# Kernel optimization log

Hardware: AMD Instinct MI355X
Metric: run time of the kernel (lower is better)

## Reference

```python
import jax, jax.numpy as jnp
import numpy as np

DIM = 768
N_HEADS = 12
HEAD_DIM = DIM // N_HEADS
HIDDEN = int(DIM * 4.0)
EPS = 1e-6


def setup_inputs() -> dict:
    key = jax.random.key(0)
    ks = jax.random.split(key, 12)
    s = 0.02
    return {
        "x": jax.random.normal(ks[0], (4, 2048, DIM), dtype=jnp.float32),
        "ln1_g": jnp.ones((DIM,), jnp.float32),
        "ln1_b": jnp.zeros((DIM,), jnp.float32),
        "qkv_w": jax.random.normal(ks[1], (3 * DIM, DIM), jnp.float32) * s,
        "qkv_b": jnp.zeros((3 * DIM,), jnp.float32),
        "proj_w": jax.random.normal(ks[2], (DIM, DIM), jnp.float32) * s,
        "proj_b": jnp.zeros((DIM,), jnp.float32),
        "ln2_g": jnp.ones((DIM,), jnp.float32),
        "ln2_b": jnp.zeros((DIM,), jnp.float32),
        "fc1_w": jax.random.normal(ks[3], (HIDDEN, DIM), jnp.float32) * s,
        "fc1_b": jnp.zeros((HIDDEN,), jnp.float32),
        "fc2_w": jax.random.normal(ks[4], (DIM, HIDDEN), jnp.float32) * s,
        "fc2_b": jnp.zeros((DIM,), jnp.float32),
    }


def layer_norm(x, g, b):
    mu = jnp.mean(x, axis=-1, keepdims=True)
    var = jnp.mean(jnp.square(x - mu), axis=-1, keepdims=True)
    return (x - mu) * jax.lax.rsqrt(var + EPS) * g + b


def reference(x, ln1_g, ln1_b, qkv_w, qkv_b, proj_w, proj_b,
              ln2_g, ln2_b, fc1_w, fc1_b, fc2_w, fc2_b):
    B, N, D = x.shape
    # --- attention branch ---
    h = layer_norm(x, ln1_g, ln1_b)
    qkv = h @ qkv_w.T + qkv_b                      # [B, N, 3D]
    qkv = qkv.reshape(B, N, 3, N_HEADS, HEAD_DIM).transpose(2, 0, 3, 1, 4)
    q, k, v = qkv[0], qkv[1], qkv[2]               # each [B, H, N, d]
    scale = HEAD_DIM ** -0.5
    scores = jnp.einsum("bhqd,bhkd->bhqk", q, k) * scale
    attn = jax.nn.softmax(scores, axis=-1)
    out = jnp.einsum("bhqk,bhkd->bhqd", attn, v)   # [B, H, N, d]
    out = out.transpose(0, 2, 1, 3).reshape(B, N, D)
    x = x + (out @ proj_w.T + proj_b)
    # --- MLP branch ---
    h = layer_norm(x, ln2_g, ln2_b)
    h = jax.nn.gelu(h @ fc1_w.T + fc1_b, approximate=False)
    x = x + (h @ fc2_w.T + fc2_b)
    return x
```

## Files before the change

kernel.cpp:

```cpp
#include <hip/hip_runtime.h>


#define DIM    768
#define NHEAD  12
#define HDIM   64
#define HID    3072
#define BATCH  4
#define SEQ    2048
#define MTOT   (BATCH * SEQ)
#define D3     (3 * DIM)

#define QSCALE 0.18033688011112042f
#define GELU_K 2.30220816f

typedef short bf16x8 __attribute__((ext_vector_type(8)));
typedef float f32x4  __attribute__((ext_vector_type(4)));

__device__ __forceinline__ float exp2fast(float x) {
    return __builtin_amdgcn_exp2f(x);
}

__device__ __forceinline__ float gelu_f(float v) {
    float y = v * (1.f + 0.044715f * v * v) * GELU_K;
    float t = exp2fast(fminf(y, 30.f));
#if __has_builtin(__builtin_amdgcn_rcpf)
    return v * t * __builtin_amdgcn_rcpf(t + 1.f);
#else
    return v * t / (t + 1.f);
#endif
}

__device__ __forceinline__ short f2bf(float f) {
    union { float f; unsigned u; } c; c.f = f;
    unsigned r = c.u + 0x7FFFu + ((c.u >> 16) & 1u);
    return (short)(r >> 16);
}

__device__ __forceinline__ short4 pk4bf(float a, float b, float c, float d) {
#if __has_builtin(__builtin_amdgcn_cvt_pk_bf16_f32)
    auto lo = __builtin_amdgcn_cvt_pk_bf16_f32(a, b);
    auto hi = __builtin_amdgcn_cvt_pk_bf16_f32(c, d);
    union { decltype(lo) v; int i; } ul, uh;
    ul.v = lo; uh.v = hi;
    short4 r;
    *(int*)&r.x = ul.i; *(int*)&r.z = uh.i;
    return r;
#else
    return make_short4(f2bf(a), f2bf(b), f2bf(c), f2bf(d));
#endif
}

__device__ __forceinline__ void gld_lds16(const short* g, short* l) {
    __builtin_amdgcn_global_load_lds(
        (const __attribute__((address_space(1))) unsigned int*)g,
        (__attribute__((address_space(3))) unsigned int*)l, 16, 0, 0);
}

__global__ __launch_bounds__(256) void tobf4_k(
    const float* __restrict__ s0, short* __restrict__ d0, int n0,
    const float* __restrict__ s1, short* __restrict__ d1, int n1,
    const float* __restrict__ s2, short* __restrict__ d2, int n2,
    const float* __restrict__ s3, short* __restrict__ d3, int n3)
{
    int i = blockIdx.x * 256 + threadIdx.x;
    const float* s; short* d;
    if (i < n0)                { s = s0; d = d0; }
    else if ((i -= n0) < n1)   { s = s1; d = d1; }
    else if ((i -= n1) < n2)   { s = s2; d = d2; }
    else if ((i -= n2) < n3)   { s = s3; d = d3; }
    else return;
    float4 v = ((const float4*)s)[i];
    ((short4*)d)[i] = pk4bf(v.x, v.y, v.z, v.w);
}

__global__ __launch_bounds__(256) void ln_k(
    const float* __restrict__ x, const float* __restrict__ g,
    const float* __restrict__ bta, short* __restrict__ y)
{
    __shared__ float sb[2][4];
    const int row = blockIdx.x, tid = threadIdx.x;
    const float* xr = x + (size_t)row * DIM;
    float v0 = xr[tid], v1 = xr[tid + 256], v2 = xr[tid + 512];
    float s = v0 + v1 + v2;
    #pragma unroll
    for (int o = 32; o; o >>= 1) s += __shfl_down(s, o);
    if ((tid & 63) == 0) sb[0][tid >> 6] = s;
    __syncthreads();
    float mu = (sb[0][0] + sb[0][1] + sb[0][2] + sb[0][3]) * (1.f / DIM);
    float d0 = v0 - mu, d1 = v1 - mu, d2 = v2 - mu;
    float q = d0 * d0 + d1 * d1 + d2 * d2;
    #pragma unroll
    for (int o = 32; o; o >>= 1) q += __shfl_down(q, o);
    if ((tid & 63) == 0) sb[1][tid >> 6] = q;
    __syncthreads();
    float var = (sb[1][0] + sb[1][1] + sb[1][2] + sb[1][3]) * (1.f / DIM);
    float inv = rsqrtf(var + 1e-6f);
    short* yr = y + (size_t)row * DIM;
    yr[tid]       = f2bf(d0 * inv * g[tid]       + bta[tid]);
    yr[tid + 256] = f2bf(d1 * inv * g[tid + 256] + bta[tid + 256]);
    yr[tid + 512] = f2bf(d2 * inv * g[tid + 512] + bta[tid + 512]);
}

template<int BN, int WM, int WN, int TM, int TN, int MODE>
__global__ __launch_bounds__(256) void gemm_bt(
    const short* __restrict__ A, const short* __restrict__ W,
    const float* __restrict__ bias, const float* __restrict__ resid,
    void* __restrict__ Cout, short* __restrict__ vt,
    int M, int N, int K)
{
    __shared__ __align__(16) short smem[2 * 128 * 32 + 2 * BN * 32];
    short (*A0)[32] = (short(*)[32])smem;
    short (*A1)[32] = (short(*)[32])(smem + 128 * 32);
    short (*B0)[32] = (short(*)[32])(smem + 2 * 128 * 32);
    short (*B1)[32] = (short(*)[32])(smem + 2 * 128 * 32 + BN * 32);

    const int tid = threadIdx.x, lane = tid & 63, wv = tid >> 6;
    const int bm = blockIdx.y << 7;
    const int bn = blockIdx.x * BN;
    const int wmo = (wv / WN) * (TM * 16);
    const int wno = (wv % WN) * (TN * 16);
    const int l15 = lane & 15, quad = lane >> 4;

    const int srow = lane >> 2;
    const int scol = (lane & 3) << 3;

    f32x4 acc[TM][TN] = {};

    for (int k0 = 0; k0 < K; k0 += 64) {
        __syncthreads();
        #pragma unroll
        for (int p = 0; p < 2; ++p) {
            const int rs = wv * 16 + p * 64;
            const short* ga = A + (size_t)(bm + rs + srow) * K + k0 + scol;
            gld_lds16(ga,      &A0[rs][0]);
            gld_lds16(ga + 32, &A1[rs][0]);
        }
        #pragma unroll
        for (int p = 0; p < BN / 64; ++p) {
            const int rs = wv * 16 + p * 64;
            const short* gw = W + (size_t)(bn + rs + srow) * K + k0 + scol;
            gld_lds16(gw,      &B0[rs][0]);
            gld_lds16(gw + 32, &B1[rs][0]);
        }
        __syncthreads();

        #pragma unroll
        for (int ks = 0; ks < 2; ++ks) {
            short (*As)[32] = ks ? A1 : A0;
            short (*Bs)[32] = ks ? B1 : B0;
            bf16x8 af[TM], bfr[TN];
            #pragma unroll
            for (int t = 0; t < TM; ++t)
                af[t] = *(const bf16x8*)&As[wmo + t * 16 + l15][quad << 3];
            #pragma unroll
            for (int u = 0; u < TN; ++u)
                bfr[u] = *(const bf16x8*)&Bs[wno + u * 16 + l15][quad << 3];
            #pragma unroll
            for (int t = 0; t < TM; ++t)
                #pragma unroll
                for (int u = 0; u < TN; ++u)
                    acc[t][u] = __builtin_amdgcn_mfma_f32_16x16x32_bf16(
                        af[t], bfr[u], acc[t][u], 0, 0, 0);
        }
    }

    if (MODE == 3 && bn >= 1536) {
        short (*Tr)[136] = (short(*)[136])smem;
        #pragma unroll 1
        for (int half = 0; half < 2; ++half) {
            __syncthreads();
            if ((wno >> 6) == half) {
                #pragma unroll
                for (int u = 0; u < TN; ++u) {
                    const float bv = bias[bn + half * 64 + u * 16 + l15];
                    #pragma unroll
                    for (int t = 0; t < TM; ++t)
                        *(short4*)&Tr[u * 16 + l15][wmo + t * 16 + (quad << 2)] =
                            pk4bf(acc[t][u][0] + bv, acc[t][u][1] + bv,
                                  acc[t][u][2] + bv, acc[t][u][3] + bv);
                }
            }
            __syncthreads();
            const int dd = tid >> 2, seg = (tid & 3) << 5;
            const int col = bn + half * 64 + dd;
            const int hh = (col - 1536) >> 6, d = (col - 1536) & 63;
            const int b = bm >> 11, n0 = (bm & 2047) + seg;
            short* dst = &vt[((((size_t)b * NHEAD + hh) << 6) + d) * SEQ + n0];
            #pragma unroll
            for (int c = 0; c < 4; ++c)
                ((int4*)dst)[c] = *(const int4*)&Tr[dd][seg + (c << 3)];
        }
        return;
    }

    #pragma unroll
    for (int u = 0; u < TN; ++u) {
        const int col = bn + wno + u * 16 + l15;
        const float bv = bias[col];
        #pragma unroll
        for (int t = 0; t < TM; ++t) {
            const int row0 = bm + wmo + t * 16 + (quad << 2);
            #pragma unroll
            for (int r = 0; r < 4; ++r) {
                float v = acc[t][u][r] + bv;
                const size_t idx = (size_t)(row0 + r) * N + col;
                if (MODE == 0) {
                    ((float*)Cout)[idx] = v + resid[idx];
                } else if (MODE == 2) {
                    ((short*)Cout)[idx] = f2bf(gelu_f(v));
                } else {
                    if (col < DIM) v *= QSCALE;
                    ((short*)Cout)[idx] = f2bf(v);
                }
            }
        }
    }
}

__global__ __launch_bounds__(256) void attn_k(
    const short* __restrict__ qkv, const short* __restrict__ vt,
    short* __restrict__ out)
{
    __shared__ __align__(16) short Ks[64][72];
    __shared__ __align__(16) short Vs[64][72];
    __shared__ __align__(16) short Ps[4][32][72];

    const int bh = blockIdx.x, b = bh / NHEAD, h = bh % NHEAD;
    const int qb = blockIdx.y;
    const int tid = threadIdx.x, lane = tid & 63, wv = tid >> 6;
    const int l15 = lane & 15, quad = lane >> 4;

    const size_t qbase = (size_t)b * SEQ * D3;
    const size_t vbase = (((size_t)bh) << 6) * SEQ;

    bf16x8 qf[2][2];
    #pragma unroll
    for (int tm = 0; tm < 2; ++tm) {
        const int m = (qb << 7) + wv * 32 + tm * 16 + l15;
        #pragma unroll
        for (int ks = 0; ks < 2; ++ks)
            qf[tm][ks] = *(const bf16x8*)&qkv[qbase + (size_t)m * D3 + h * HDIM
                                             + ks * 32 + (quad << 3)];
    }

    float psum[2] = {0.f, 0.f};
    f32x4 acc[2][4] = {};

    const int srow = tid >> 3;
    const int scol = (tid & 7) << 3;

    for (int kb = 0; kb < SEQ / 64; ++kb) {
        __syncthreads();
        #pragma unroll
        for (int p = 0; p < 2; ++p) {
            const int r = srow + p * 32;
            *(int4*)&Ks[r][scol] = *(const int4*)&qkv[qbase
                + (size_t)((kb << 6) + r) * D3 + DIM + h * HDIM + scol];
            *(int4*)&Vs[r][scol] = *(const int4*)&vt[vbase
                + (size_t)r * SEQ + (kb << 6) + scol];
        }
        __syncthreads();

        f32x4 st[2][4] = {};
        #pragma unroll
        for (int kt = 0; kt < 4; ++kt)
            #pragma unroll
            for (int ks = 0; ks < 2; ++ks) {
                bf16x8 kf = *(const bf16x8*)&Ks[kt * 16 + l15][ks * 32 + (quad << 3)];
                #pragma unroll
                for (int tm = 0; tm < 2; ++tm)
                    st[tm][kt] = __builtin_amdgcn_mfma_f32_16x16x32_bf16(
                        kf, qf[tm][ks], st[tm][kt], 0, 0, 0);
            }

        #pragma unroll
        for (int tm = 0; tm < 2; ++tm) {
            #pragma unroll
            for (int kt = 0; kt < 4; ++kt) {
                const float p0 = exp2fast(st[tm][kt][0]);
                const float p1 = exp2fast(st[tm][kt][1]);
                const float p2 = exp2fast(st[tm][kt][2]);
                const float p3 = exp2fast(st[tm][kt][3]);
                psum[tm] += (p0 + p1) + (p2 + p3);
                *(short4*)&Ps[wv][tm * 16 + l15][kt * 16 + (quad << 2)] =
                    pk4bf(p0, p1, p2, p3);
            }
        }

        #pragma unroll
        for (int ks = 0; ks < 2; ++ks) {
            bf16x8 pf[2];
            #pragma unroll
            for (int tm = 0; tm < 2; ++tm)
                pf[tm] = *(const bf16x8*)&Ps[wv][tm * 16 + l15][ks * 32 + (quad << 3)];
            #pragma unroll
            for (int u = 0; u < 4; ++u) {
                bf16x8 vf = *(const bf16x8*)&Vs[u * 16 + l15][ks * 32 + (quad << 3)];
                #pragma unroll
                for (int tm = 0; tm < 2; ++tm)
                    acc[tm][u] = __builtin_amdgcn_mfma_f32_16x16x32_bf16(
                        vf, pf[tm], acc[tm][u], 0, 0, 0);
            }
        }
    }

    #pragma unroll
    for (int tm = 0; tm < 2; ++tm) {
        psum[tm] += __shfl_xor(psum[tm], 16);
        psum[tm] += __shfl_xor(psum[tm], 32);
    }

    #pragma unroll
    for (int tm = 0; tm < 2; ++tm) {
        const float inv = 1.f / psum[tm];
        const int q = (qb << 7) + wv * 32 + tm * 16 + l15;
        #pragma unroll
        for (int u = 0; u < 4; ++u) {
            const int d0 = u * 16 + (quad << 2);
            *(short4*)&out[((size_t)b * SEQ + q) * DIM + h * HDIM + d0] =
                pk4bf(acc[tm][u][0] * inv, acc[tm][u][1] * inv,
                      acc[tm][u][2] * inv, acc[tm][u][3] * inv);
        }
    }
}

extern "C" void kernel_launch(void* const* d_in, const int* in_sizes, int n_in,
                              void* d_out, int out_size, void* d_ws, size_t ws_size,
                              hipStream_t stream) {
    const float* x      = (const float*)d_in[0];
    const float* ln1_g  = (const float*)d_in[1];
    const float* ln1_b  = (const float*)d_in[2];
    const float* qkv_w  = (const float*)d_in[3];
    const float* qkv_b  = (const float*)d_in[4];
    const float* proj_w = (const float*)d_in[5];
    const float* proj_b = (const float*)d_in[6];
    const float* ln2_g  = (const float*)d_in[7];
    const float* ln2_b  = (const float*)d_in[8];
    const float* fc1_w  = (const float*)d_in[9];
    const float* fc1_b  = (const float*)d_in[10];
    const float* fc2_w  = (const float*)d_in[11];
    const float* fc2_b  = (const float*)d_in[12];
    float* out = (float*)d_out;

    short* ws16 = (short*)d_ws;
    short* wqkv = ws16;
    short* wprj = wqkv + (size_t)D3 * DIM;
    short* wf1  = wprj + (size_t)DIM * DIM;
    short* wf2  = wf1  + (size_t)HID * DIM;
    short* h    = wf2  + (size_t)DIM * HID;
    short* big  = h    + (size_t)MTOT * DIM;
    short* vtb  = big  + (size_t)MTOT * HID;
    float* x2   = (float*)(vtb + (size_t)MTOT * DIM);

    dim3 blk(256);

    const int n0 = (D3 * DIM) / 4, n1 = (DIM * DIM) / 4,
              n2 = (HID * DIM) / 4, n3 = (DIM * HID) / 4;
    tobf4_k<<<(n0 + n1 + n2 + n3 + 255) / 256, blk, 0, stream>>>(
        qkv_w, wqkv, n0, proj_w, wprj, n1, fc1_w, wf1, n2, fc2_w, wf2, n3);

    ln_k<<<MTOT, blk, 0, stream>>>(x, ln1_g, ln1_b, h);
    gemm_bt<128, 2, 2, 4, 4, 3><<<dim3(D3 / 128, MTOT / 128), blk, 0, stream>>>(
        h, wqkv, qkv_b, nullptr, big, vtb, MTOT, D3, DIM);
    attn_k<<<dim3(BATCH * NHEAD, SEQ / 128), blk, 0, stream>>>(big, vtb, h);
    gemm_bt<64, 4, 1, 2, 4, 0><<<dim3(DIM / 64, MTOT / 128), blk, 0, stream>>>(
        h, wprj, proj_b, x, x2, nullptr, MTOT, DIM, DIM);
    ln_k<<<MTOT, blk, 0, stream>>>(x2, ln2_g, ln2_b, vtb);
    gemm_bt<128, 2, 2, 4, 4, 2><<<dim3(HID / 128, MTOT / 128), blk, 0, stream>>>(
        vtb, wf1, fc1_b, nullptr, big, nullptr, MTOT, HID, DIM);
    gemm_bt<64, 4, 1, 2, 4, 0><<<dim3(DIM / 64, MTOT / 128), blk, 0, stream>>>(
        big, wf2, fc2_b, x2, out, nullptr, MTOT, DIM, HID);
}
```

Measured before the change: 431.1 us.

## Replace GEMM with 256x128-tile, 8-wave, double-buffered swizzled-LDS kernel

Replaces the templated 128xBN GEMM with a single 512-thread kernel that computes 256x128 output tiles. It double-buffers LDS so the next K-slice loads while MFMAs run, and XOR-swizzles the LDS layout to avoid bank conflicts. It also raises wave priority around MFMA issue. The V-transpose epilogue now writes short4 directly from registers instead of staging through LDS. The risks are lower occupancy from 96KB of LDS per block, and fewer blocks for the 768-wide projection GEMMs (only 6x32 tiles), which could hurt load balance.

```diff
diff --git a/kernel.cpp b/kernel.cpp
--- a/kernel.cpp
+++ b/kernel.cpp
@@ -37,17 +37,12 @@
 }
 
 __device__ __forceinline__ short4 pk4bf(float a, float b, float c, float d) {
-#if __has_builtin(__builtin_amdgcn_cvt_pk_bf16_f32)
-    auto lo = __builtin_amdgcn_cvt_pk_bf16_f32(a, b);
-    auto hi = __builtin_amdgcn_cvt_pk_bf16_f32(c, d);
-    union { decltype(lo) v; int i; } ul, uh;
-    ul.v = lo; uh.v = hi;
+    int lo, hi;
+    asm("v_cvt_pk_bf16_f32 %0, %1, %2" : "=v"(lo) : "v"(a), "v"(b));
+    asm("v_cvt_pk_bf16_f32 %0, %1, %2" : "=v"(hi) : "v"(c), "v"(d));
     short4 r;
-    *(int*)&r.x = ul.i; *(int*)&r.z = uh.i;
+    *(int*)&r.x = lo; *(int*)&r.z = hi;
     return r;
-#else
-    return make_short4(f2bf(a), f2bf(b), f2bf(c), f2bf(d));
-#endif
 }
 
 __device__ __forceinline__ void gld_lds16(const short* g, short* l) {
@@ -101,108 +96,113 @@
     yr[tid + 512] = f2bf(d2 * inv * g[tid + 512] + bta[tid + 512]);
 }
 
-template<int BN, int WM, int WN, int TM, int TN, int MODE>
-__global__ __launch_bounds__(256) void gemm_bt(
+template<int MODE>
+__global__ __launch_bounds__(512) void gemm8_k(
     const short* __restrict__ A, const short* __restrict__ W,
     const float* __restrict__ bias, const float* __restrict__ resid,
     void* __restrict__ Cout, short* __restrict__ vt,
     int M, int N, int K)
 {
-    __shared__ __align__(16) short smem[2 * 128 * 32 + 2 * BN * 32];
-    short (*A0)[32] = (short(*)[32])smem;
-    short (*A1)[32] = (short(*)[32])(smem + 128 * 32);
-    short (*B0)[32] = (short(*)[32])(smem + 2 * 128 * 32);
-    short (*B1)[32] = (short(*)[32])(smem + 2 * 128 * 32 + BN * 32);
+    __shared__ __align__(16) short sm[2][24576];
 
     const int tid = threadIdx.x, lane = tid & 63, wv = tid >> 6;
-    const int bm = blockIdx.y << 7;
-    const int bn = blockIdx.x * BN;
-    const int wmo = (wv / WN) * (TM * 16);
-    const int wno = (wv % WN) * (TN * 16);
     const int l15 = lane & 15, quad = lane >> 4;
-
-    const int srow = lane >> 2;
-    const int scol = (lane & 3) << 3;
-
-    f32x4 acc[TM][TN] = {};
-
-    for (int k0 = 0; k0 < K; k0 += 64) {
-        __syncthreads();
-        #pragma unroll
-        for (int p = 0; p < 2; ++p) {
-            const int rs = wv * 16 + p * 64;
-            const short* ga = A + (size_t)(bm + rs + srow) * K + k0 + scol;
-            gld_lds16(ga,      &A0[rs][0]);
-            gld_lds16(ga + 32, &A1[rs][0]);
-        }
-        #pragma unroll
-        for (int p = 0; p < BN / 64; ++p) {
-            const int rs = wv * 16 + p * 64;
-            const short* gw = W + (size_t)(bn + rs + srow) * K + k0 + scol;
-            gld_lds16(gw,      &B0[rs][0]);
-            gld_lds16(gw + 32, &B1[rs][0]);
-        }
-        __syncthreads();
+    const int bm = blockIdx.y << 8, bn = blockIdx.x << 7;
+
+    const int srow  = lane >> 3;
+    const int chunk = (lane & 7) ^ srow;
+    const int arow  = wv * 8 + srow;
+
+    const short* Ag = A + (size_t)(bm + arow) * K + chunk * 8;
+    const short* Wg = W + (size_t)(bn + arow) * K + chunk * 8;
+
+    const int nt = K >> 6;
+
+    auto stage = [&](short* s, int k0) {
+        #pragma unroll
+        for (int u = 0; u < 2; ++u)
+            #pragma unroll
+            for (int i = 0; i < 2; ++i)
+                gld_lds16(Ag + k0 + (size_t)(u * 128 + i * 64) * K,
+                          s + u * 8192 + i * 4096 + wv * 512);
+        #pragma unroll
+        for (int i = 0; i < 2; ++i)
+            gld_lds16(Wg + k0 + (size_t)(i * 64) * K,
+                      s + 16384 + i * 4096 + wv * 512);
+    };
+
+    f32x4 acc[4][4] = {};
+    stage(&sm[0][0], 0);
+
+    const int rsel = (wv >> 1) * 64;
+    const int csel = (wv & 1) * 64;
+    const int xorr = (l15 & 7) << 4;
+
+    for (int t = 0; t < nt; ++t) {
+        const short* Sc = &sm[t & 1][0];
+        asm volatile("s_waitcnt vmcnt(0)" ::: "memory");
+        __builtin_amdgcn_s_barrier();
+        __builtin_amdgcn_sched_barrier(0);
+        const int kn = (t + 1 < nt ? t + 1 : t) << 6;
+        stage(&sm[(t + 1) & 1][0], kn);
 
         #pragma unroll
         for (int ks = 0; ks < 2; ++ks) {
-            short (*As)[32] = ks ? A1 : A0;
-            short (*Bs)[32] = ks ? B1 : B0;
-            bf16x8 af[TM], bfr[TN];
-            #pragma unroll
-            for (int t = 0; t < TM; ++t)
-                af[t] = *(const bf16x8*)&As[wmo + t * 16 + l15][quad << 3];
-            #pragma unroll
-            for (int u = 0; u < TN; ++u)
-                bfr[u] = *(const bf16x8*)&Bs[wno + u * 16 + l15][quad << 3];
-            #pragma unroll
-            for (int t = 0; t < TM; ++t)
+            bf16x8 af[4], bfr[4];
+            #pragma unroll
+            for (int mf = 0; mf < 4; ++mf) {
+                const int row = rsel + mf * 16 + l15;
+                const int off = (row >> 7) * 16384 + ((row & 127) << 7)
+                              + (((ks << 6) + (quad << 4)) ^ xorr);
+                af[mf] = *(const bf16x8*)((const char*)Sc + off);
+            }
+            #pragma unroll
+            for (int nf = 0; nf < 4; ++nf) {
+                const int brow = csel + nf * 16 + l15;
+                const int off = 32768 + (brow << 7)
+                              + (((ks << 6) + (quad << 4)) ^ xorr);
+                bfr[nf] = *(const bf16x8*)((const char*)Sc + off);
+            }
+            __builtin_amdgcn_s_setprio(1);
+            #pragma unroll
+            for (int mf = 0; mf < 4; ++mf)
                 #pragma unroll
-                for (int u = 0; u < TN; ++u)
-                    acc[t][u] = __builtin_amdgcn_mfma_f32_16x16x32_bf16(
-                        af[t], bfr[u], acc[t][u], 0, 0, 0);
+                for (int nf = 0; nf < 4; ++nf)
+                    acc[mf][nf] = __builtin_amdgcn_mfma_f32_16x16x32_bf16(
+                        af[mf], bfr[nf], acc[mf][nf], 0, 0, 0);
+            __builtin_amdgcn_s_setprio(0);
         }
     }
 
     if (MODE == 3 && bn >= 1536) {
-        short (*Tr)[136] = (short(*)[136])smem;
-        #pragma unroll 1
-        for (int half = 0; half < 2; ++half) {
-            __syncthreads();
-            if ((wno >> 6) == half) {
-                #pragma unroll
-                for (int u = 0; u < TN; ++u) {
-                    const float bv = bias[bn + half * 64 + u * 16 + l15];
-                    #pragma unroll
-                    for (int t = 0; t < TM; ++t)
-                        *(short4*)&Tr[u * 16 + l15][wmo + t * 16 + (quad << 2)] =
-                            pk4bf(acc[t][u][0] + bv, acc[t][u][1] + bv,
-                                  acc[t][u][2] + bv, acc[t][u][3] + bv);
-                }
-            }
-            __syncthreads();
-            const int dd = tid >> 2, seg = (tid & 3) << 5;
-            const int col = bn + half * 64 + dd;
-            const int hh = (col - 1536) >> 6, d = (col - 1536) & 63;
-            const int b = bm >> 11, n0 = (bm & 2047) + seg;
-            short* dst = &vt[((((size_t)b * NHEAD + hh) << 6) + d) * SEQ + n0];
-            #pragma unroll
-            for (int c = 0; c < 4; ++c)
-                ((int4*)dst)[c] = *(const int4*)&Tr[dd][seg + (c << 3)];
+        const size_t bbase = (size_t)(bm >> 11) * NHEAD;
+        #pragma unroll
+        for (int nf = 0; nf < 4; ++nf) {
+            const int col = bn + csel + nf * 16 + l15;
+            const float bv = bias[col];
+            const int d = col - 1536, hh = d >> 6, dd = d & 63;
+            const size_t vrow = (((bbase + hh) << 6) + dd) * SEQ;
+            #pragma unroll
+            for (int mf = 0; mf < 4; ++mf) {
+                const int n0 = (bm & 2047) + rsel + mf * 16 + (quad << 2);
+                *(short4*)&vt[vrow + n0] =
+                    pk4bf(acc[mf][nf][0] + bv, acc[mf][nf][1] + bv,
+                          acc[mf][nf][2] + bv, acc[mf][nf][3] + bv);
+            }
         }
         return;
     }
 
     #pragma unroll
-    for (int u = 0; u < TN; ++u) {
-        const int col = bn + wno + u * 16 + l15;
+    for (int nf = 0; nf < 4; ++nf) {
+        const int col = bn + csel + nf * 16 + l15;
         const float bv = bias[col];
         #pragma unroll
-        for (int t = 0; t < TM; ++t) {
-            const int row0 = bm + wmo + t * 16 + (quad << 2);
+        for (int mf = 0; mf < 4; ++mf) {
+            const int row0 = bm + rsel + mf * 16 + (quad << 2);
             #pragma unroll
             for (int r = 0; r < 4; ++r) {
-                float v = acc[t][u][r] + bv;
+                float v = acc[mf][nf][r] + bv;
                 const size_t idx = (size_t)(row0 + r) * N + col;
                 if (MODE == 0) {
                     ((float*)Cout)[idx] = v + resid[idx];
@@ -360,14 +360,14 @@
         qkv_w, wqkv, n0, proj_w, wprj, n1, fc1_w, wf1, n2, fc2_w, wf2, n3);
 
     ln_k<<<MTOT, blk, 0, stream>>>(x, ln1_g, ln1_b, h);
-    gemm_bt<128, 2, 2, 4, 4, 3><<<dim3(D3 / 128, MTOT / 128), blk, 0, stream>>>(
+    gemm8_k<3><<<dim3(D3 / 128, MTOT / 256), 512, 0, stream>>>(
         h, wqkv, qkv_b, nullptr, big, vtb, MTOT, D3, DIM);
     attn_k<<<dim3(BATCH * NHEAD, SEQ / 128), blk, 0, stream>>>(big, vtb, h);
-    gemm_bt<64, 4, 1, 2, 4, 0><<<dim3(DIM / 64, MTOT / 128), blk, 0, stream>>>(
+    gemm8_k<0><<<dim3(DIM / 128, MTOT / 256), 512, 0, stream>>>(
         h, wprj, proj_b, x, x2, nullptr, MTOT, DIM, DIM);
     ln_k<<<MTOT, blk, 0, stream>>>(x2, ln2_g, ln2_b, vtb);
-    gemm_bt<128, 2, 2, 4, 4, 2><<<dim3(HID / 128, MTOT / 128), blk, 0, stream>>>(
+    gemm8_k<2><<<dim3(HID / 128, MTOT / 256), 512, 0, stream>>>(
         vtb, wf1, fc1_b, nullptr, big, nullptr, MTOT, HID, DIM);
-    gemm_bt<64, 4, 1, 2, 4, 0><<<dim3(DIM / 64, MTOT / 128), blk, 0, stream>>>(
+    gemm8_k<0><<<dim3(DIM / 128, MTOT / 256), 512, 0, stream>>>(
         big, wf2, fc2_b, x2, out, nullptr, MTOT, DIM, HID);
 }
```

Measured after the change: 391.3 us. -9.2%, faster.
